# Performance work log

Measured on AMD Instinct MI355X. Metric: run time of the kernel, lower is better.

## Reference

```python
import jax, jax.numpy as jnp
import numpy as np

D_MODEL = 512
N_HEADS = 8
D_Q = 64   # d_queries == d_keys
D_V = 64
LN_EPS = 1e-5


def setup_inputs() -> dict:
    key = jax.random.key(0)
    ks = jax.random.split(key, 10)
    N, S = 4, 2048
    x = jax.random.normal(ks[0], (N, S, D_MODEL), dtype=jnp.float32)
    lengths = jax.random.randint(ks[1], (N,), 1, S + 1)  # true lengths in [1, S]
    s = 0.02
    Wq = jax.random.normal(ks[2], (D_MODEL, N_HEADS * D_Q), dtype=jnp.float32) * s
    bq = jnp.zeros((N_HEADS * D_Q,), dtype=jnp.float32)
    Wkv = jax.random.normal(ks[3], (D_MODEL, N_HEADS * (D_Q + D_V)), dtype=jnp.float32) * s
    bkv = jnp.zeros((N_HEADS * (D_Q + D_V),), dtype=jnp.float32)
    Wo = jax.random.normal(ks[4], (N_HEADS * D_V, D_MODEL), dtype=jnp.float32) * s
    bo = jnp.zeros((D_MODEL,), dtype=jnp.float32)
    gamma = jnp.ones((D_MODEL,), dtype=jnp.float32)
    beta = jnp.zeros((D_MODEL,), dtype=jnp.float32)
    return {"x": x, "key_value_sequence_lengths": lengths, "Wq": Wq, "bq": bq,
            "Wkv": Wkv, "bkv": bkv, "Wo": Wo, "bo": bo, "gamma": gamma, "beta": beta}


def reference(x, key_value_sequence_lengths, Wq, bq, Wkv, bkv, Wo, bo, gamma, beta):
    # Decoder self-attention: query_sequences == key_value_sequences == x.
    N, S, _ = x.shape
    H, dq, dv = N_HEADS, D_Q, D_V

    residual = x
    # Pre-LayerNorm (applied to both queries and keys/values since self-attention)
    mu = jnp.mean(x, axis=-1, keepdims=True)
    var = jnp.var(x, axis=-1, keepdims=True)
    xn = (x - mu) * jax.lax.rsqrt(var + LN_EPS) * gamma + beta

    q = (xn @ Wq + bq).reshape(N, S, H, dq).transpose(0, 2, 1, 3)          # (N,H,S,dq)
    kv = xn @ Wkv + bkv
    k = kv[..., : H * dq].reshape(N, S, H, dq).transpose(0, 2, 1, 3)       # (N,H,S,dq)
    v = kv[..., H * dq :].reshape(N, S, H, dv).transpose(0, 2, 1, 3)       # (N,H,S,dv)

    scores = jnp.einsum("nhqd,nhkd->nhqk", q, k) / jnp.sqrt(jnp.float32(dq))  # (N,H,S,S)

    # Padding mask over keys + causal (not-future) mask
    key_pos = jnp.arange(S)
    pad_ok = key_pos[None, None, None, :] < key_value_sequence_lengths[:, None, None, None]
    causal_ok = (key_pos[None, :] <= jnp.arange(S)[:, None])[None, None, :, :]
    mask = pad_ok & causal_ok
    scores = jnp.where(mask, scores, -jnp.inf)

    attn = jax.nn.softmax(scores, axis=-1)
    out = jnp.einsum("nhqk,nhkd->nqhd", attn, v).reshape(N, S, H * dv)
    out = out @ Wo + bo
    return out + residual
```

## Files before the change

kernel.cpp:

```cpp
#include <hip/hip_runtime.h>
#include <hip/hip_bf16.h>

typedef __attribute__((ext_vector_type(4))) float f32x4;
typedef __attribute__((ext_vector_type(16))) float f32x16;
typedef __attribute__((ext_vector_type(8))) short short8;

#define D_MODEL 512
#define SQ 2048
#define NH 8
#define NBATCH 4
#define MROWS (NBATCH * SQ)

#define CHUNKS_PER_NH 72
#define NSLOTS (32 * CHUNKS_PER_NH)

__device__ __forceinline__ ushort f2b(float x) {
  unsigned int u = __float_as_uint(x);
  return (ushort)((u + 0x7fffu + ((u >> 16) & 1u)) >> 16);
}

__device__ __forceinline__ f32x4 mfma16(short8 a, short8 b, f32x4 c) {
  return __builtin_amdgcn_mfma_f32_16x16x32_bf16(a, b, c, 0, 0, 0);
}
__device__ __forceinline__ f32x16 mfma32(short8 a, short8 b, f32x16 c) {
  return __builtin_amdgcn_mfma_f32_32x32x16_bf16(a, b, c, 0, 0, 0);
}

#define GLOAD_LDS16(g, l)                                                      \
  __builtin_amdgcn_global_load_lds(                                            \
      (const __attribute__((address_space(1))) unsigned int*)(g),              \
      (__attribute__((address_space(3))) unsigned int*)(l), 16, 0, 0)

__global__ __launch_bounds__(256) void transpose_w(const float* __restrict__ W,
                                                   ushort* __restrict__ WT,
                                                   int K, int N) {
  __shared__ ushort tile[32][33];
  int n0 = blockIdx.x * 32, k0 = blockIdx.y * 32;
  int tx = threadIdx.x & 31, ty = threadIdx.x >> 5;
#pragma unroll
  for (int i = 0; i < 4; ++i) {
    int k = ty + i * 8;
    tile[tx][k] = f2b(W[(size_t)(k0 + k) * N + n0 + tx]);
  }
  __syncthreads();
#pragma unroll
  for (int i = 0; i < 4; ++i) {
    int nn = ty + i * 8;
    WT[(size_t)(n0 + nn) * K + k0 + tx] = tile[nn][tx];
  }
}

__global__ __launch_bounds__(256) void ln_kernel(const float* __restrict__ x,
                                                 const float* __restrict__ gamma,
                                                 const float* __restrict__ beta,
                                                 ushort* __restrict__ xn) {
  int wid = threadIdx.x >> 6, lane = threadIdx.x & 63;
  int row = blockIdx.x * 4 + wid;
  const float4* xr = (const float4*)(x + (size_t)row * D_MODEL);
  float4 v0 = xr[lane];
  float4 v1 = xr[lane + 64];
  float s = v0.x + v0.y + v0.z + v0.w + v1.x + v1.y + v1.z + v1.w;
  float q = v0.x * v0.x + v0.y * v0.y + v0.z * v0.z + v0.w * v0.w +
            v1.x * v1.x + v1.y * v1.y + v1.z * v1.z + v1.w * v1.w;
#pragma unroll
  for (int m = 1; m < 64; m <<= 1) {
    s += __shfl_xor(s, m, 64);
    q += __shfl_xor(q, m, 64);
  }
  float mu = s * (1.f / 512.f);
  float var = q * (1.f / 512.f) - mu * mu;
  float rs = rsqrtf(var + 1e-5f);
  const float4* g4 = (const float4*)gamma;
  const float4* b4 = (const float4*)beta;
  ushort* out = xn + (size_t)row * D_MODEL;
#pragma unroll
  for (int i = 0; i < 2; ++i) {
    float4 v = i ? v1 : v0;
    float4 gg = g4[lane + i * 64];
    float4 bb = b4[lane + i * 64];
    ushort4 o;
    o.x = f2b((v.x - mu) * rs * gg.x + bb.x);
    o.y = f2b((v.y - mu) * rs * gg.y + bb.y);
    o.z = f2b((v.z - mu) * rs * gg.z + bb.z);
    o.w = f2b((v.w - mu) * rs * gg.w + bb.w);
    *(ushort4*)(out + (lane + i * 64) * 4) = o;
  }
}

__global__ __launch_bounds__(256) void qkv_gemm(
    const ushort* __restrict__ A, const ushort* __restrict__ BT,
    const float* __restrict__ bq, const float* __restrict__ bkv,
    ushort* __restrict__ qbuf, ushort* __restrict__ kvbuf, float qscale) {
  __shared__ __align__(16) ushort As[128 * 32];
  __shared__ __align__(16) ushort Bs[128 * 32];
  const int tid = threadIdx.x, lane = tid & 63, wid = tid >> 6;
  const int g = lane >> 4, r = lane & 15;
  const int wr = wid >> 1, wc = wid & 1;
  const int bm = blockIdx.y * 128, bn = blockIdx.x * 128;

  f32x4 acc[4][4];
#pragma unroll
  for (int a = 0; a < 4; ++a)
#pragma unroll
    for (int b = 0; b < 4; ++b) acc[a][b] = (f32x4){0.f, 0.f, 0.f, 0.f};

  const int srow = 32 * wid + (lane >> 2);
  const int scol = (lane & 3) * 8;
  const ushort* ga = A + (size_t)(bm + srow) * 512 + scol;
  const ushort* gb = BT + (size_t)(bn + srow) * 512 + scol;
  ushort* la = As + 32 * 32 * wid;
  ushort* lb = Bs + 32 * 32 * wid;

  for (int kb = 0; kb < 512; kb += 32) {
    __syncthreads();
    GLOAD_LDS16(ga + kb, la);
    GLOAD_LDS16(ga + kb + 16 * 512, la + 16 * 32);
    GLOAD_LDS16(gb + kb, lb);
    GLOAD_LDS16(gb + kb + 16 * 512, lb + 16 * 32);
    __syncthreads();
    short8 af[4], bf[4];
#pragma unroll
    for (int i2 = 0; i2 < 4; ++i2) {
      af[i2] = *(const short8*)&As[(wr * 64 + i2 * 16 + r) * 32 + g * 8];
      bf[i2] = *(const short8*)&Bs[(wc * 64 + i2 * 16 + r) * 32 + g * 8];
    }
#pragma unroll
    for (int a = 0; a < 4; ++a)
#pragma unroll
      for (int b = 0; b < 4; ++b) acc[a][b] = mfma16(af[a], bf[b], acc[a][b]);
  }

  const bool isQ = (bn < 512);
  const float* bias = isQ ? bq : bkv;
  ushort* dst = isQ ? qbuf : kvbuf;
  const int cb = isQ ? bn : bn - 512;
  const size_t stride = isQ ? 512 : 1024;
  const float scale = isQ ? qscale : 1.0f;

#pragma unroll
  for (int a = 0; a < 4; ++a) {
#pragma unroll
    for (int reg = 0; reg < 4; ++reg) {
      int row = bm + wr * 64 + a * 16 + g * 4 + reg;
#pragma unroll
      for (int b = 0; b < 4; ++b) {
        int col = cb + wc * 64 + b * 16 + r;
        dst[(size_t)row * stride + col] = f2b((acc[a][b][reg] + bias[col]) * scale);
      }
    }
  }
}

__global__ __launch_bounds__(256) void o_gemm(
    const ushort* __restrict__ A, const ushort* __restrict__ BT,
    const float* __restrict__ bias, const float* __restrict__ resid,
    float* __restrict__ outF) {
  __shared__ __align__(16) ushort As[128 * 32];
  __shared__ __align__(16) ushort Bs[128 * 32];
  const int tid = threadIdx.x, lane = tid & 63, wid = tid >> 6;
  const int g = lane >> 4, r = lane & 15;
  const int wr = wid >> 1, wc = wid & 1;
  const int bm = blockIdx.y * 128, bn = blockIdx.x * 128;

  f32x4 acc[4][4];
#pragma unroll
  for (int a = 0; a < 4; ++a)
#pragma unroll
    for (int b = 0; b < 4; ++b) acc[a][b] = (f32x4){0.f, 0.f, 0.f, 0.f};

  const int srow = 32 * wid + (lane >> 2);
  const int scol = (lane & 3) * 8;
  const ushort* ga = A + (size_t)(bm + srow) * 512 + scol;
  const ushort* gb = BT + (size_t)(bn + srow) * 512 + scol;
  ushort* la = As + 32 * 32 * wid;
  ushort* lb = Bs + 32 * 32 * wid;

  for (int kb = 0; kb < 512; kb += 32) {
    __syncthreads();
    GLOAD_LDS16(ga + kb, la);
    GLOAD_LDS16(ga + kb + 16 * 512, la + 16 * 32);
    GLOAD_LDS16(gb + kb, lb);
    GLOAD_LDS16(gb + kb + 16 * 512, lb + 16 * 32);
    __syncthreads();
    short8 af[4], bf[4];
#pragma unroll
    for (int i2 = 0; i2 < 4; ++i2) {
      af[i2] = *(const short8*)&As[(wr * 64 + i2 * 16 + r) * 32 + g * 8];
      bf[i2] = *(const short8*)&Bs[(wc * 64 + i2 * 16 + r) * 32 + g * 8];
    }
#pragma unroll
    for (int a = 0; a < 4; ++a)
#pragma unroll
      for (int b = 0; b < 4; ++b) acc[a][b] = mfma16(af[a], bf[b], acc[a][b]);
  }

#pragma unroll
  for (int a = 0; a < 4; ++a) {
#pragma unroll
    for (int reg = 0; reg < 4; ++reg) {
      int row = bm + wr * 64 + a * 16 + g * 4 + reg;
#pragma unroll
      for (int b = 0; b < 4; ++b) {
        int col = bn + wc * 64 + b * 16 + r;
        outF[(size_t)row * 512 + col] =
            acc[a][b][reg] + bias[col] + resid[(size_t)row * 512 + col];
      }
    }
  }
}

__global__ __launch_bounds__(256) void attn_kernel(
    const ushort* __restrict__ qbuf, const ushort* __restrict__ kvbuf,
    const int* __restrict__ lengths, ushort* __restrict__ partialO,
    float2* __restrict__ mlbuf) {
  __shared__ __align__(16) ushort smem[9728];

  const int tid = threadIdx.x, lane = tid & 63, wid = tid >> 6;
  const int l31 = lane & 31, h = lane >> 5;

  const int bid = blockIdx.x;
  const int xcd = bid & 7;
  const int j = bid >> 3;
  const int grp = j / 72;
  const int L = j - grp * 72;
  const int nh = (grp << 3) | xcd;
  const int n = nh >> 3, head = nh & 7;
  int qi = 0, c = L;
  while (c >= ((qi + 2) >> 1)) { c -= (qi + 2) >> 1; ++qi; }
  const int T = 4 * qi + 4, nch = (qi + 2) >> 1;
  const int t0 = (c * T) / nch;
  const int t1 = ((c + 1) * T) / nch;
  const int slot = nh * CHUNKS_PER_NH + L;

  const int qb = qi * 128;
  const int len = lengths[n];
  const int q0w = qb + 32 * wid;
  const int q_own = q0w + l31;
  const int nt_w_abs = 4 * qi + wid + 1;
  const int tlen = (len + 31) >> 5;
  int nt = min(t1, tlen) - t0;
  if (nt < 0) nt = 0;

  f32x16 o0, o1;
#pragma unroll
  for (int i = 0; i < 16; ++i) { o0[i] = 0.f; o1[i] = 0.f; }
  float m_ = -1e30f, ls = 0.f;

  const int skey = tid >> 3, sc8 = tid & 7;
  const int kp = lane & 15, dvb = wid * 4 + (lane >> 4);
  const int mu = (l31 >> 2) & 3;

  int voff[4];
#pragma unroll
  for (int jj = 0; jj < 4; ++jj) {
    int dv = 4 * dvb + jj;
    voff[jj] = dv * 20 + (((kp >> 2) ^ ((dv >> 2) & 3)) << 2) + (kp & 3);
  }

  const ushort* kvbase = kvbuf + (size_t)n * SQ * 1024 + head * 64;
  const ushort* kSrc = kvbase + (size_t)(t0 * 32 + skey) * 1024 + sc8 * 8;
  const ushort* vSrc = kvbase + 512 + (size_t)(t0 * 32 + 2 * kp) * 1024 + dvb * 4;
  const int kLdsOff = skey * 72 + sc8 * 8;

  if (nt > 0) {
    short8 qf[4];
    {
      const ushort* qp = qbuf + (size_t)(n * SQ + q_own) * 512 + head * 64 + 8 * h;
#pragma unroll
      for (int kc = 0; kc < 4; ++kc) qf[kc] = *(const short8*)(qp + 16 * kc);
    }

    uint4 kA, kB = {};
    uint2 vaA, vbA, vaB = {}, vbB = {};
    kA = *(const uint4*)kSrc;
    vaA = *(const uint2*)vSrc;
    vbA = *(const uint2*)(vSrc + 1024);
    kSrc += 32 * 1024;
    vSrc += 32 * 1024;
    if (nt > 1) {
      kB = *(const uint4*)kSrc;
      vaB = *(const uint2*)vSrc;
      vbB = *(const uint2*)(vSrc + 1024);
      kSrc += 32 * 1024;
      vSrc += 32 * 1024;
    }
    {
      *(uint4*)(smem + kLdsOff) = kA;
      const ushort* a16 = (const ushort*)&vaA;
      const ushort* b16 = (const ushort*)&vbA;
#pragma unroll
      for (int jj = 0; jj < 4; ++jj)
        ((unsigned*)(smem + 4608))[voff[jj]] =
            (unsigned)a16[jj] | ((unsigned)b16[jj] << 16);
    }
    __syncthreads();

    for (int i = 0; i < nt; ++i) {
      const int t = t0 + i;
      const int cur = i & 1;
      if (i + 2 < nt) {
        if (cur == 0) {
          kA = *(const uint4*)kSrc;
          vaA = *(const uint2*)vSrc;
          vbA = *(const uint2*)(vSrc + 1024);
        } else {
          kB = *(const uint4*)kSrc;
          vaB = *(const uint2*)vSrc;
          vbB = *(const uint2*)(vSrc + 1024);
        }
        kSrc += 32 * 1024;
        vSrc += 32 * 1024;
      }

      if (t < nt_w_abs) {
        const int kb = t * 32;
        const ushort* KtB = smem + cur * 2304;
        const ushort* VtB = smem + 4608 + cur * 2560;

        f32x16 s;
#pragma unroll
        for (int i2 = 0; i2 < 16; ++i2) s[i2] = 0.f;
        {
          const ushort* kr_ = KtB + l31 * 72 + 8 * h;
          short8 k0 = *(const short8*)(kr_);
          short8 k1 = *(const short8*)(kr_ + 16);
          short8 k2 = *(const short8*)(kr_ + 32);
          short8 k3 = *(const short8*)(kr_ + 48);
          s = mfma32(k0, qf[0], s);
          s = mfma32(k1, qf[1], s);
          s = mfma32(k2, qf[2], s);
          s = mfma32(k3, qf[3], s);
        }

        if (kb + 31 > q0w || kb + 31 >= len) {
          int keyb = kb + 4 * h;
#pragma unroll
          for (int reg = 0; reg < 16; ++reg) {
            int key = keyb + (reg & 3) + 8 * (reg >> 2);
            bool ok = (key <= q_own) && (key < len);
            s[reg] = ok ? s[reg] : -1e30f;
          }
        }

        float a0 = fmaxf(fmaxf(s[0], s[1]), s[2]);
        float a1 = fmaxf(fmaxf(s[3], s[4]), s[5]);
        float a2 = fmaxf(fmaxf(s[6], s[7]), s[8]);
        float a3 = fmaxf(fmaxf(s[9], s[10]), s[11]);
        float a4 = fmaxf(fmaxf(s[12], s[13]), s[14]);
        float mx = fmaxf(fmaxf(fmaxf(a0, a1), s[15]),
                         fmaxf(fmaxf(a2, a3), a4));
        {
          auto rr = __builtin_amdgcn_permlane32_swap(__float_as_uint(mx),
                                                     __float_as_uint(mx), false, false);
          mx = fmaxf(__uint_as_float(((const unsigned*)&rr)[0]),
                     __uint_as_float(((const unsigned*)&rr)[1]));
        }

        if (!__all(mx <= m_ + 8.0f)) {
          float mn = fmaxf(m_, mx);
          float sf = __builtin_amdgcn_exp2f(m_ - mn);
          m_ = mn;
          ls *= sf;
#pragma unroll
          for (int i2 = 0; i2 < 16; ++i2) { o0[i2] *= sf; o1[i2] *= sf; }
        }

        float p[16];
#pragma unroll
        for (int reg = 0; reg < 16; ++reg)
          p[reg] = __builtin_amdgcn_exp2f(s[reg] - m_);

        float rsum = ((p[0] + p[1]) + (p[2] + p[3])) + ((p[4] + p[5]) + (p[6] + p[7])) +
                     ((p[8] + p[9]) + (p[10] + p[11])) +
                     ((p[12] + p[13]) + (p[14] + p[15]));
        {
          auto rr = __builtin_amdgcn_permlane32_swap(__float_as_uint(rsum),
                                                     __float_as_uint(rsum), false, false);
          rsum = __uint_as_float(((const unsigned*)&rr)[0]) +
                 __uint_as_float(((const unsigned*)&rr)[1]);
        }
        ls += rsum;

        unsigned pk[8];
#pragma unroll
        for (int jj = 0; jj < 8; ++jj)
          pk[jj] = __builtin_amdgcn_perm(__float_as_uint(p[2 * jj + 1]),
                                         __float_as_uint(p[2 * jj]), 0x07060302u);

#pragma unroll
        for (int kc = 0; kc < 2; ++kc) {
          short8 pf;
          ((unsigned*)&pf)[0] = pk[4 * kc + 0];
          ((unsigned*)&pf)[1] = pk[4 * kc + 1];
          ((unsigned*)&pf)[2] = pk[4 * kc + 2];
          ((unsigned*)&pf)[3] = pk[4 * kc + 3];
          const int u0 = ((2 * kc) ^ mu) << 3;
          const ushort* vb0 = VtB + l31 * 40 + 4 * h;
          const ushort* vb1 = VtB + (32 + l31) * 40 + 4 * h;
          short8 vf0, vf1;
          ((uint2*)&vf0)[0] = *(const uint2*)(vb0 + u0);
          ((uint2*)&vf0)[1] = *(const uint2*)(vb0 + (u0 ^ 8));
          ((uint2*)&vf1)[0] = *(const uint2*)(vb1 + u0);
          ((uint2*)&vf1)[1] = *(const uint2*)(vb1 + (u0 ^ 8));
          o0 = mfma32(vf0, pf, o0);
          o1 = mfma32(vf1, pf, o1);
        }
      }

      if (i + 1 < nt) {
        ushort* KtN = smem + (cur ^ 1) * 2304;
        unsigned* VtN = (unsigned*)(smem + 4608 + (cur ^ 1) * 2560);
        if (cur == 0) {
          *(uint4*)(KtN + kLdsOff) = kB;
          const ushort* a16 = (const ushort*)&vaB;
          const ushort* b16 = (const ushort*)&vbB;
#pragma unroll
          for (int jj = 0; jj < 4; ++jj)
            VtN[voff[jj]] = (unsigned)a16[jj] | ((unsigned)b16[jj] << 16);
        } else {
          *(uint4*)(KtN + kLdsOff) = kA;
          const ushort* a16 = (const ushort*)&vaA;
          const ushort* b16 = (const ushort*)&vbA;
#pragma unroll
          for (int jj = 0; jj < 4; ++jj)
            VtN[voff[jj]] = (unsigned)a16[jj] | ((unsigned)b16[jj] << 16);
        }
      }
      __syncthreads();
    }
  }

  const unsigned long long alive = __ballot(ls > 0.f);
  {
    float inv = (ls > 0.f) ? 1.f / ls : 0.f;
    ushort* OtW = smem + wid * (32 * 68);
#pragma unroll
    for (int b = 0; b < 2; ++b) {
#pragma unroll
      for (int reg = 0; reg < 16; reg += 2) {
        float e0 = (b ? o1[reg] : o0[reg]) * inv;
        float e1 = (b ? o1[reg + 1] : o0[reg + 1]) * inv;
        unsigned pko = __builtin_amdgcn_perm(__float_as_uint(e1),
                                             __float_as_uint(e0), 0x07060302u);
        int dv = 32 * b + (reg & 3) + 8 * (reg >> 2) + 4 * h;
        *(unsigned*)(OtW + l31 * 68 + dv) = pko;
      }
    }
    if (h == 0) mlbuf[slot * 128 + 32 * wid + l31] = make_float2(m_, ls);
  }
  __syncthreads();
  if (alive) {
    int r = lane >> 1, sg = lane & 1;
    if ((alive >> r) & 1ULL) {
      const ushort* rp = smem + wid * (32 * 68) + r * 68 + sg * 32;
      uint2 d0 = *(const uint2*)(rp);
      uint2 d1 = *(const uint2*)(rp + 4);
      uint2 d2 = *(const uint2*)(rp + 8);
      uint2 d3 = *(const uint2*)(rp + 12);
      uint2 d4 = *(const uint2*)(rp + 16);
      uint2 d5 = *(const uint2*)(rp + 20);
      uint2 d6 = *(const uint2*)(rp + 24);
      uint2 d7 = *(const uint2*)(rp + 28);
      ushort* gp = partialO + (size_t)slot * 8192 + (32 * wid + r) * 64 + sg * 32;
      *(uint4*)(gp) = make_uint4(d0.x, d0.y, d1.x, d1.y);
      *(uint4*)(gp + 8) = make_uint4(d2.x, d2.y, d3.x, d3.y);
      *(uint4*)(gp + 16) = make_uint4(d4.x, d4.y, d5.x, d5.y);
      *(uint4*)(gp + 24) = make_uint4(d6.x, d6.y, d7.x, d7.y);
    }
  }
}

__global__ __launch_bounds__(256) void attn_combine(
    const ushort* __restrict__ partialO, const float2* __restrict__ mlbuf,
    ushort* __restrict__ attout) {
  const int bx = blockIdx.x;
  const int nh = bx >> 4, qi = bx & 15;
  const int nch = (qi + 2) >> 1;
  const int off = (qi * (qi + 2) + (qi & 1)) >> 2;
  const int n = nh >> 3, head = nh & 7;
  const int slot0 = nh * CHUNKS_PER_NH + off;

  const int tid = threadIdx.x;
  const int r = tid >> 1, half = tid & 1;

  float mstar = -1e30f;
  for (int c = 0; c < nch; ++c) {
    float2 ml = mlbuf[(slot0 + c) * 128 + r];
    mstar = fmaxf(mstar, ml.x);
  }

  float acc[32];
#pragma unroll
  for (int j = 0; j < 32; ++j) acc[j] = 0.f;
  float Lsum = 0.f;

  for (int c = 0; c < nch; ++c) {
    float2 ml = mlbuf[(slot0 + c) * 128 + r];
    if (ml.y > 0.f) {
      float cf = ml.y * __builtin_amdgcn_exp2f(ml.x - mstar);
      Lsum += cf;
      const uint4* p =
          (const uint4*)(partialO + (size_t)(slot0 + c) * 8192 + r * 64 + half * 32);
#pragma unroll
      for (int u = 0; u < 4; ++u) {
        uint4 d = p[u];
        unsigned w[4] = {d.x, d.y, d.z, d.w};
#pragma unroll
        for (int k = 0; k < 4; ++k) {
          acc[u * 8 + 2 * k] += cf * __uint_as_float(w[k] << 16);
          acc[u * 8 + 2 * k + 1] += cf * __uint_as_float(w[k] & 0xffff0000u);
        }
      }
    }
  }

  const float inv = 1.f / Lsum;
  uint4 outw[4];
#pragma unroll
  for (int u = 0; u < 4; ++u) {
    unsigned ww[4];
#pragma unroll
    for (int k = 0; k < 4; ++k) {
      float e0 = acc[u * 8 + 2 * k] * inv;
      float e1 = acc[u * 8 + 2 * k + 1] * inv;
      ww[k] = ((unsigned)f2b(e0)) | (((unsigned)f2b(e1)) << 16);
    }
    outw[u] = make_uint4(ww[0], ww[1], ww[2], ww[3]);
  }
  ushort* gp = attout + (size_t)(n * SQ + qi * 128 + r) * 512 + head * 64 + half * 32;
#pragma unroll
  for (int u = 0; u < 4; ++u) ((uint4*)gp)[u] = outw[u];
}

extern "C" void kernel_launch(void* const* d_in, const int* in_sizes, int n_in,
                              void* d_out, int out_size, void* d_ws, size_t ws_size,
                              hipStream_t stream) {
  const float* x = (const float*)d_in[0];
  const int* lens = (const int*)d_in[1];
  const float* Wq = (const float*)d_in[2];
  const float* bq = (const float*)d_in[3];
  const float* Wkv = (const float*)d_in[4];
  const float* bkv = (const float*)d_in[5];
  const float* Wo = (const float*)d_in[6];
  const float* bo = (const float*)d_in[7];
  const float* gamma = (const float*)d_in[8];
  const float* beta = (const float*)d_in[9];
  float* out = (float*)d_out;

  size_t off = 0;
  auto alloc = [&](size_t bytes) {
    void* p = (char*)d_ws + off;
    off += (bytes + 255) & ~(size_t)255;
    return p;
  };
  ushort* xn = (ushort*)alloc((size_t)MROWS * 512 * 2);
  ushort* qbuf = (ushort*)alloc((size_t)MROWS * 512 * 2);
  ushort* kvbuf = (ushort*)alloc((size_t)MROWS * 1024 * 2);
  ushort* WT = (ushort*)alloc((size_t)1536 * 512 * 2);
  ushort* WoT = (ushort*)alloc((size_t)512 * 512 * 2);
  ushort* partialO = (ushort*)alloc((size_t)NSLOTS * 8192 * 2);
  float2* mlbuf = (float2*)alloc((size_t)NSLOTS * 128 * 8);
  ushort* attout = xn;

  transpose_w<<<dim3(16, 16), 256, 0, stream>>>(Wq, WT, 512, 512);
  transpose_w<<<dim3(32, 16), 256, 0, stream>>>(Wkv, WT + 512 * 512, 512, 1024);
  transpose_w<<<dim3(16, 16), 256, 0, stream>>>(Wo, WoT, 512, 512);

  ln_kernel<<<MROWS / 4, 256, 0, stream>>>(x, gamma, beta, xn);

  qkv_gemm<<<dim3(12, 64), 256, 0, stream>>>(xn, WT, bq, bkv, qbuf, kvbuf,
                                             0.125f * 1.44269504f);

  attn_kernel<<<dim3(NSLOTS), 256, 0, stream>>>(qbuf, kvbuf, lens, partialO, mlbuf);
  attn_combine<<<dim3(512), 256, 0, stream>>>(partialO, mlbuf, attout);

  o_gemm<<<dim3(4, 64), 256, 0, stream>>>(attout, WoT, bo, x, out);
}
```

Measured before the change: 123.9 us.

## Load K fragments directly from global into registers, bypassing LDS staging

```diff
diff --git a/kernel.cpp b/kernel.cpp
--- a/kernel.cpp
+++ b/kernel.cpp
@@ -213,7 +213,7 @@
     const ushort* __restrict__ qbuf, const ushort* __restrict__ kvbuf,
     const int* __restrict__ lengths, ushort* __restrict__ partialO,
     float2* __restrict__ mlbuf) {
-  __shared__ __align__(16) ushort smem[9728];
+  __shared__ __align__(16) ushort smem[8704];
 
   const int tid = threadIdx.x, lane = tid & 63, wid = tid >> 6;
   const int l31 = lane & 31, h = lane >> 5;
@@ -246,7 +246,6 @@
   for (int i = 0; i < 16; ++i) { o0[i] = 0.f; o1[i] = 0.f; }
   float m_ = -1e30f, ls = 0.f;
 
-  const int skey = tid >> 3, sc8 = tid & 7;
   const int kp = lane & 15, dvb = wid * 4 + (lane >> 4);
   const int mu = (l31 >> 2) & 3;
 
@@ -258,9 +257,8 @@
   }
 
   const ushort* kvbase = kvbuf + (size_t)n * SQ * 1024 + head * 64;
-  const ushort* kSrc = kvbase + (size_t)(t0 * 32 + skey) * 1024 + sc8 * 8;
+  const ushort* kRow = kvbase + (size_t)(t0 * 32 + l31) * 1024 + 8 * h;
   const ushort* vSrc = kvbase + 512 + (size_t)(t0 * 32 + 2 * kp) * 1024 + dvb * 4;
-  const int kLdsOff = skey * 72 + sc8 * 8;
 
   if (nt > 0) {
     short8 qf[4];
@@ -270,27 +268,20 @@
       for (int kc = 0; kc < 4; ++kc) qf[kc] = *(const short8*)(qp + 16 * kc);
     }
 
-    uint4 kA, kB = {};
-    uint2 vaA, vbA, vaB = {}, vbB = {};
-    kA = *(const uint4*)kSrc;
-    vaA = *(const uint2*)vSrc;
-    vbA = *(const uint2*)(vSrc + 1024);
-    kSrc += 32 * 1024;
+    short8 kfA[4], kfB[4];
+    uint2 va, vb;
+#pragma unroll
+    for (int kc = 0; kc < 4; ++kc) kfA[kc] = *(const short8*)(kRow + 16 * kc);
+    kRow += 32 * 1024;
+    va = *(const uint2*)vSrc;
+    vb = *(const uint2*)(vSrc + 1024);
     vSrc += 32 * 1024;
-    if (nt > 1) {
-      kB = *(const uint4*)kSrc;
-      vaB = *(const uint2*)vSrc;
-      vbB = *(const uint2*)(vSrc + 1024);
-      kSrc += 32 * 1024;
-      vSrc += 32 * 1024;
-    }
     {
-      *(uint4*)(smem + kLdsOff) = kA;
-      const ushort* a16 = (const ushort*)&vaA;
-      const ushort* b16 = (const ushort*)&vbA;
+      const ushort* a16 = (const ushort*)&va;
+      const ushort* b16 = (const ushort*)&vb;
 #pragma unroll
       for (int jj = 0; jj < 4; ++jj)
-        ((unsigned*)(smem + 4608))[voff[jj]] =
+        ((unsigned*)smem)[voff[jj]] =
             (unsigned)a16[jj] | ((unsigned)b16[jj] << 16);
     }
     __syncthreads();
@@ -298,39 +289,31 @@
     for (int i = 0; i < nt; ++i) {
       const int t = t0 + i;
       const int cur = i & 1;
-      if (i + 2 < nt) {
-        if (cur == 0) {
-          kA = *(const uint4*)kSrc;
-          vaA = *(const uint2*)vSrc;
-          vbA = *(const uint2*)(vSrc + 1024);
-        } else {
-          kB = *(const uint4*)kSrc;
-          vaB = *(const uint2*)vSrc;
-          vbB = *(const uint2*)(vSrc + 1024);
-        }
-        kSrc += 32 * 1024;
+      const bool more = (i + 1 < nt);
+      uint2 va2, vb2;
+      if (more) {
+        va2 = *(const uint2*)vSrc;
+        vb2 = *(const uint2*)(vSrc + 1024);
         vSrc += 32 * 1024;
+        if (t + 1 < nt_w_abs) {
+#pragma unroll
+          for (int kc = 0; kc < 4; ++kc)
+            kfB[kc] = *(const short8*)(kRow + 16 * kc);
+        }
+        kRow += 32 * 1024;
       }
 
       if (t < nt_w_abs) {
         const int kb = t * 32;
-        const ushort* KtB = smem + cur * 2304;
-        const ushort* VtB = smem + 4608 + cur * 2560;
+        const ushort* VtB = smem + cur * 2560;
 
         f32x16 s;
 #pragma unroll
         for (int i2 = 0; i2 < 16; ++i2) s[i2] = 0.f;
-        {
-          const ushort* kr_ = KtB + l31 * 72 + 8 * h;
-          short8 k0 = *(const short8*)(kr_);
-          short8 k1 = *(const short8*)(kr_ + 16);
-          short8 k2 = *(const short8*)(kr_ + 32);
-          short8 k3 = *(const short8*)(kr_ + 48);
-          s = mfma32(k0, qf[0], s);
-          s = mfma32(k1, qf[1], s);
-          s = mfma32(k2, qf[2], s);
-          s = mfma32(k3, qf[3], s);
-        }
+        s = mfma32(kfA[0], qf[0], s);
+        s = mfma32(kfA[1], qf[1], s);
+        s = mfma32(kfA[2], qf[2], s);
+        s = mfma32(kfA[3], qf[3], s);
 
         if (kb + 31 > q0w || kb + 31 >= len) {
           int keyb = kb + 4 * h;
@@ -407,24 +390,15 @@
         }
       }
 
-      if (i + 1 < nt) {
-        ushort* KtN = smem + (cur ^ 1) * 2304;
-        unsigned* VtN = (unsigned*)(smem + 4608 + (cur ^ 1) * 2560);
-        if (cur == 0) {
-          *(uint4*)(KtN + kLdsOff) = kB;
-          const ushort* a16 = (const ushort*)&vaB;
-          const ushort* b16 = (const ushort*)&vbB;
-#pragma unroll
-          for (int jj = 0; jj < 4; ++jj)
-            VtN[voff[jj]] = (unsigned)a16[jj] | ((unsigned)b16[jj] << 16);
-        } else {
-          *(uint4*)(KtN + kLdsOff) = kA;
-          const ushort* a16 = (const ushort*)&vaA;
-          const ushort* b16 = (const ushort*)&vbA;
-#pragma unroll
-          for (int jj = 0; jj < 4; ++jj)
-            VtN[voff[jj]] = (unsigned)a16[jj] | ((unsigned)b16[jj] << 16);
-        }
+      if (more) {
+        unsigned* VtN = (unsigned*)smem + (cur ^ 1) * 1280;
+        const ushort* a16 = (const ushort*)&va2;
+        const ushort* b16 = (const ushort*)&vb2;
+#pragma unroll
+        for (int jj = 0; jj < 4; ++jj)
+          VtN[voff[jj]] = (unsigned)a16[jj] | ((unsigned)b16[jj] << 16);
+#pragma unroll
+        for (int kc = 0; kc < 4; ++kc) kfA[kc] = kfB[kc];
       }
       __syncthreads();
     }
```

Measured after the change: 142.2 us. 14.8% more time.

## Process two KV tiles per attention loop iteration with doubled LDS staging

Applied to the files above, without the earlier changes.

```diff
diff --git a/kernel.cpp b/kernel.cpp
--- a/kernel.cpp
+++ b/kernel.cpp
@@ -213,7 +213,7 @@
     const ushort* __restrict__ qbuf, const ushort* __restrict__ kvbuf,
     const int* __restrict__ lengths, ushort* __restrict__ partialO,
     float2* __restrict__ mlbuf) {
-  __shared__ __align__(16) ushort smem[9728];
+  __shared__ __align__(16) ushort smem[19456];
 
   const int tid = threadIdx.x, lane = tid & 63, wid = tid >> 6;
   const int l31 = lane & 31, h = lane >> 5;
@@ -227,9 +227,9 @@
   const int n = nh >> 3, head = nh & 7;
   int qi = 0, c = L;
   while (c >= ((qi + 2) >> 1)) { c -= (qi + 2) >> 1; ++qi; }
-  const int T = 4 * qi + 4, nch = (qi + 2) >> 1;
-  const int t0 = (c * T) / nch;
-  const int t1 = ((c + 1) * T) / nch;
+  const int P = 2 * qi + 2, nch = (qi + 2) >> 1;
+  const int t0 = 2 * ((c * P) / nch);
+  const int t1 = 2 * (((c + 1) * P) / nch);
   const int slot = nh * CHUNKS_PER_NH + L;
 
   const int qb = qi * 128;
@@ -240,6 +240,7 @@
   const int tlen = (len + 31) >> 5;
   int nt = min(t1, tlen) - t0;
   if (nt < 0) nt = 0;
+  const int np = (nt + 1) >> 1;
 
   f32x16 o0, o1;
 #pragma unroll
@@ -270,66 +271,212 @@
       for (int kc = 0; kc < 4; ++kc) qf[kc] = *(const short8*)(qp + 16 * kc);
     }
 
-    uint4 kA, kB = {};
-    uint2 vaA, vbA, vaB = {}, vbB = {};
-    kA = *(const uint4*)kSrc;
+    uint4 kra, krb;
+    uint2 vaA, vbA, vaB, vbB;
+    kra = *(const uint4*)kSrc;
+    krb = *(const uint4*)(kSrc + 32 * 1024);
     vaA = *(const uint2*)vSrc;
     vbA = *(const uint2*)(vSrc + 1024);
-    kSrc += 32 * 1024;
-    vSrc += 32 * 1024;
-    if (nt > 1) {
-      kB = *(const uint4*)kSrc;
-      vaB = *(const uint2*)vSrc;
-      vbB = *(const uint2*)(vSrc + 1024);
-      kSrc += 32 * 1024;
-      vSrc += 32 * 1024;
-    }
+    vaB = *(const uint2*)(vSrc + 32 * 1024);
+    vbB = *(const uint2*)(vSrc + 33 * 1024);
+    kSrc += 64 * 1024;
+    vSrc += 64 * 1024;
     {
-      *(uint4*)(smem + kLdsOff) = kA;
+      *(uint4*)(smem + kLdsOff) = kra;
+      *(uint4*)(smem + 2304 + kLdsOff) = krb;
+      unsigned* V0 = (unsigned*)(smem + 9216);
+      unsigned* V1 = V0 + 1280;
       const ushort* a16 = (const ushort*)&vaA;
       const ushort* b16 = (const ushort*)&vbA;
-#pragma unroll
-      for (int jj = 0; jj < 4; ++jj)
-        ((unsigned*)(smem + 4608))[voff[jj]] =
-            (unsigned)a16[jj] | ((unsigned)b16[jj] << 16);
+      const ushort* c16 = (const ushort*)&vaB;
+      const ushort* d16 = (const ushort*)&vbB;
+#pragma unroll
+      for (int jj = 0; jj < 4; ++jj) {
+        V0[voff[jj]] = (unsigned)a16[jj] | ((unsigned)b16[jj] << 16);
+        V1[voff[jj]] = (unsigned)c16[jj] | ((unsigned)d16[jj] << 16);
+      }
     }
     __syncthreads();
 
-    for (int i = 0; i < nt; ++i) {
-      const int t = t0 + i;
+    for (int i = 0; i < np; ++i) {
+      const int tA = t0 + 2 * i, tB = tA + 1;
       const int cur = i & 1;
-      if (i + 2 < nt) {
-        if (cur == 0) {
-          kA = *(const uint4*)kSrc;
-          vaA = *(const uint2*)vSrc;
-          vbA = *(const uint2*)(vSrc + 1024);
-        } else {
-          kB = *(const uint4*)kSrc;
-          vaB = *(const uint2*)vSrc;
-          vbB = *(const uint2*)(vSrc + 1024);
-        }
-        kSrc += 32 * 1024;
-        vSrc += 32 * 1024;
+      const bool more = (i + 1 < np);
+      if (more) {
+        kra = *(const uint4*)kSrc;
+        krb = *(const uint4*)(kSrc + 32 * 1024);
+        vaA = *(const uint2*)vSrc;
+        vbA = *(const uint2*)(vSrc + 1024);
+        vaB = *(const uint2*)(vSrc + 32 * 1024);
+        vbB = *(const uint2*)(vSrc + 33 * 1024);
+        kSrc += 64 * 1024;
+        vSrc += 64 * 1024;
       }
-
-      if (t < nt_w_abs) {
-        const int kb = t * 32;
-        const ushort* KtB = smem + cur * 2304;
-        const ushort* VtB = smem + 4608 + cur * 2560;
-
+      const bool condA = (tA < nt_w_abs);
+      const bool condB = (tB < nt_w_abs) && (2 * i + 1 < nt);
+      const ushort* KtA = smem + cur * 4608;
+      const ushort* KtB = KtA + 2304;
+      const ushort* VtA = smem + 9216 + cur * 5120;
+      const ushort* VtB = VtA + 2560;
+
+      if (condB) {
+        const int kbA = tA * 32, kbB = kbA + 32;
+        f32x16 s, s2;
+#pragma unroll
+        for (int i2 = 0; i2 < 16; ++i2) { s[i2] = 0.f; s2[i2] = 0.f; }
+        {
+          const ushort* krA_ = KtA + l31 * 72 + 8 * h;
+          const ushort* krB_ = KtB + l31 * 72 + 8 * h;
+          short8 a0 = *(const short8*)(krA_);
+          short8 a1 = *(const short8*)(krA_ + 16);
+          short8 a2 = *(const short8*)(krA_ + 32);
+          short8 a3 = *(const short8*)(krA_ + 48);
+          short8 b0 = *(const short8*)(krB_);
+          short8 b1 = *(const short8*)(krB_ + 16);
+          short8 b2 = *(const short8*)(krB_ + 32);
+          short8 b3 = *(const short8*)(krB_ + 48);
+          __builtin_amdgcn_s_setprio(1);
+          s = mfma32(a0, qf[0], s);
+          s2 = mfma32(b0, qf[0], s2);
+          s = mfma32(a1, qf[1], s);
+          s2 = mfma32(b1, qf[1], s2);
+          s = mfma32(a2, qf[2], s);
+          s2 = mfma32(b2, qf[2], s2);
+          s = mfma32(a3, qf[3], s);
+          s2 = mfma32(b3, qf[3], s2);
+          __builtin_amdgcn_s_setprio(0);
+        }
+
+        if (kbA + 31 > q0w || kbA + 31 >= len) {
+          int keyb = kbA + 4 * h;
+#pragma unroll
+          for (int reg = 0; reg < 16; ++reg) {
+            int key = keyb + (reg & 3) + 8 * (reg >> 2);
+            bool ok = (key <= q_own) && (key < len);
+            s[reg] = ok ? s[reg] : -1e30f;
+          }
+        }
+        if (kbB + 31 > q0w || kbB + 31 >= len) {
+          int keyb = kbB + 4 * h;
+#pragma unroll
+          for (int reg = 0; reg < 16; ++reg) {
+            int key = keyb + (reg & 3) + 8 * (reg >> 2);
+            bool ok = (key <= q_own) && (key < len);
+            s2[reg] = ok ? s2[reg] : -1e30f;
+          }
+        }
+
+        float m0 = fmaxf(fmaxf(s[0], s[1]), fmaxf(s[2], s[3]));
+        float m1 = fmaxf(fmaxf(s[4], s[5]), fmaxf(s[6], s[7]));
+        float m2 = fmaxf(fmaxf(s[8], s[9]), fmaxf(s[10], s[11]));
+        float m3 = fmaxf(fmaxf(s[12], s[13]), fmaxf(s[14], s[15]));
+        float m4 = fmaxf(fmaxf(s2[0], s2[1]), fmaxf(s2[2], s2[3]));
+        float m5 = fmaxf(fmaxf(s2[4], s2[5]), fmaxf(s2[6], s2[7]));
+        float m6 = fmaxf(fmaxf(s2[8], s2[9]), fmaxf(s2[10], s2[11]));
+        float m7 = fmaxf(fmaxf(s2[12], s2[13]), fmaxf(s2[14], s2[15]));
+        float mx = fmaxf(fmaxf(fmaxf(m0, m1), fmaxf(m2, m3)),
+                         fmaxf(fmaxf(m4, m5), fmaxf(m6, m7)));
+        {
+          auto rr = __builtin_amdgcn_permlane32_swap(__float_as_uint(mx),
+                                                     __float_as_uint(mx), false, false);
+          mx = fmaxf(__uint_as_float(((const unsigned*)&rr)[0]),
+                     __uint_as_float(((const unsigned*)&rr)[1]));
+        }
+
+        if (!__all(mx <= m_ + 8.0f)) {
+          float mn = fmaxf(m_, mx);
+          float sf = __builtin_amdgcn_exp2f(m_ - mn);
+          m_ = mn;
+          ls *= sf;
+#pragma unroll
+          for (int i2 = 0; i2 < 16; ++i2) { o0[i2] *= sf; o1[i2] *= sf; }
+        }
+
+#pragma unroll
+        for (int reg = 0; reg < 16; ++reg) {
+          s[reg] = __builtin_amdgcn_exp2f(s[reg] - m_);
+          s2[reg] = __builtin_amdgcn_exp2f(s2[reg] - m_);
+        }
+
+        float rsum = (((s[0] + s[1]) + (s[2] + s[3])) + ((s[4] + s[5]) + (s[6] + s[7]))) +
+                     (((s[8] + s[9]) + (s[10] + s[11])) +
+                      ((s[12] + s[13]) + (s[14] + s[15]))) +
+                     (((s2[0] + s2[1]) + (s2[2] + s2[3])) +
+                      ((s2[4] + s2[5]) + (s2[6] + s2[7]))) +
+                     (((s2[8] + s2[9]) + (s2[10] + s2[11])) +
+                      ((s2[12] + s2[13]) + (s2[14] + s2[15])));
+        {
+          auto rr = __builtin_amdgcn_permlane32_swap(__float_as_uint(rsum),
+                                                     __float_as_uint(rsum), false, false);
+          rsum = __uint_as_float(((const unsigned*)&rr)[0]) +
+                 __uint_as_float(((const unsigned*)&rr)[1]);
+        }
+        ls += rsum;
+
+        unsigned pkA[8], pkB[8];
+#pragma unroll
+        for (int jj = 0; jj < 8; ++jj) {
+          pkA[jj] = __builtin_amdgcn_perm(__float_as_uint(s[2 * jj + 1]),
+                                          __float_as_uint(s[2 * jj]), 0x07060302u);
+          pkB[jj] = __builtin_amdgcn_perm(__float_as_uint(s2[2 * jj + 1]),
+                                          __float_as_uint(s2[2 * jj]), 0x07060302u);
+        }
+
+        __builtin_amdgcn_s_setprio(1);
+#pragma unroll
+        for (int kc = 0; kc < 2; ++kc) {
+          short8 pf;
+          ((unsigned*)&pf)[0] = pkA[4 * kc + 0];
+          ((unsigned*)&pf)[1] = pkA[4 * kc + 1];
+          ((unsigned*)&pf)[2] = pkA[4 * kc + 2];
+          ((unsigned*)&pf)[3] = pkA[4 * kc + 3];
+          const int u0 = ((2 * kc) ^ mu) << 3;
+          const ushort* vb0 = VtA + l31 * 40 + 4 * h;
+          const ushort* vb1 = VtA + (32 + l31) * 40 + 4 * h;
+          short8 vf0, vf1;
+          ((uint2*)&vf0)[0] = *(const uint2*)(vb0 + u0);
+          ((uint2*)&vf0)[1] = *(const uint2*)(vb0 + (u0 ^ 8));
+          ((uint2*)&vf1)[0] = *(const uint2*)(vb1 + u0);
+          ((uint2*)&vf1)[1] = *(const uint2*)(vb1 + (u0 ^ 8));
+          o0 = mfma32(vf0, pf, o0);
+          o1 = mfma32(vf1, pf, o1);
+        }
+#pragma unroll
+        for (int kc = 0; kc < 2; ++kc) {
+          short8 pf;
+          ((unsigned*)&pf)[0] = pkB[4 * kc + 0];
+          ((unsigned*)&pf)[1] = pkB[4 * kc + 1];
+          ((unsigned*)&pf)[2] = pkB[4 * kc + 2];
+          ((unsigned*)&pf)[3] = pkB[4 * kc + 3];
+          const int u0 = ((2 * kc) ^ mu) << 3;
+          const ushort* vb0 = VtB + l31 * 40 + 4 * h;
+          const ushort* vb1 = VtB + (32 + l31) * 40 + 4 * h;
+          short8 vf0, vf1;
+          ((uint2*)&vf0)[0] = *(const uint2*)(vb0 + u0);
+          ((uint2*)&vf0)[1] = *(const uint2*)(vb0 + (u0 ^ 8));
+          ((uint2*)&vf1)[0] = *(const uint2*)(vb1 + u0);
+          ((uint2*)&vf1)[1] = *(const uint2*)(vb1 + (u0 ^ 8));
+          o0 = mfma32(vf0, pf, o0);
+          o1 = mfma32(vf1, pf, o1);
+        }
+        __builtin_amdgcn_s_setprio(0);
+      } else if (condA) {
+        const int kb = tA * 32;
         f32x16 s;
 #pragma unroll
         for (int i2 = 0; i2 < 16; ++i2) s[i2] = 0.f;
         {
-          const ushort* kr_ = KtB + l31 * 72 + 8 * h;
+          const ushort* kr_ = KtA + l31 * 72 + 8 * h;
           short8 k0 = *(const short8*)(kr_);
           short8 k1 = *(const short8*)(kr_ + 16);
           short8 k2 = *(const short8*)(kr_ + 32);
           short8 k3 = *(const short8*)(kr_ + 48);
+          __builtin_amdgcn_s_setprio(1);
           s = mfma32(k0, qf[0], s);
           s = mfma32(k1, qf[1], s);
           s = mfma32(k2, qf[2], s);
           s = mfma32(k3, qf[3], s);
+          __builtin_amdgcn_s_setprio(0);
         }
 
         if (kb + 31 > q0w || kb + 31 >= len) {
@@ -365,14 +512,13 @@
           for (int i2 = 0; i2 < 16; ++i2) { o0[i2] *= sf; o1[i2] *= sf; }
         }
 
-        float p[16];
 #pragma unroll
         for (int reg = 0; reg < 16; ++reg)
-          p[reg] = __builtin_amdgcn_exp2f(s[reg] - m_);
-
-        float rsum = ((p[0] + p[1]) + (p[2] + p[3])) + ((p[4] + p[5]) + (p[6] + p[7])) +
-                     ((p[8] + p[9]) + (p[10] + p[11])) +
-                     ((p[12] + p[13]) + (p[14] + p[15]));
+          s[reg] = __builtin_amdgcn_exp2f(s[reg] - m_);
+
+        float rsum = ((s[0] + s[1]) + (s[2] + s[3])) + ((s[4] + s[5]) + (s[6] + s[7])) +
+                     ((s[8] + s[9]) + (s[10] + s[11])) +
+                     ((s[12] + s[13]) + (s[14] + s[15]));
         {
           auto rr = __builtin_amdgcn_permlane32_swap(__float_as_uint(rsum),
                                                      __float_as_uint(rsum), false, false);
@@ -384,9 +530,10 @@
         unsigned pk[8];
 #pragma unroll
         for (int jj = 0; jj < 8; ++jj)
-          pk[jj] = __builtin_amdgcn_perm(__float_as_uint(p[2 * jj + 1]),
-                                         __float_as_uint(p[2 * jj]), 0x07060302u);
-
+          pk[jj] = __builtin_amdgcn_perm(__float_as_uint(s[2 * jj + 1]),
+                                         __float_as_uint(s[2 * jj]), 0x07060302u);
+
+        __builtin_amdgcn_s_setprio(1);
 #pragma unroll
         for (int kc = 0; kc < 2; ++kc) {
           short8 pf;
@@ -395,8 +542,8 @@
           ((unsigned*)&pf)[2] = pk[4 * kc + 2];
           ((unsigned*)&pf)[3] = pk[4 * kc + 3];
           const int u0 = ((2 * kc) ^ mu) << 3;
-          const ushort* vb0 = VtB + l31 * 40 + 4 * h;
-          const ushort* vb1 = VtB + (32 + l31) * 40 + 4 * h;
+          const ushort* vb0 = VtA + l31 * 40 + 4 * h;
+          const ushort* vb1 = VtA + (32 + l31) * 40 + 4 * h;
           short8 vf0, vf1;
           ((uint2*)&vf0)[0] = *(const uint2*)(vb0 + u0);
           ((uint2*)&vf0)[1] = *(const uint2*)(vb0 + (u0 ^ 8));
@@ -405,25 +552,23 @@
           o0 = mfma32(vf0, pf, o0);
           o1 = mfma32(vf1, pf, o1);
         }
+        __builtin_amdgcn_s_setprio(0);
       }
 
-      if (i + 1 < nt) {
-        ushort* KtN = smem + (cur ^ 1) * 2304;
-        unsigned* VtN = (unsigned*)(smem + 4608 + (cur ^ 1) * 2560);
-        if (cur == 0) {
-          *(uint4*)(KtN + kLdsOff) = kB;
-          const ushort* a16 = (const ushort*)&vaB;
-          const ushort* b16 = (const ushort*)&vbB;
-#pragma unroll
-          for (int jj = 0; jj < 4; ++jj)
-            VtN[voff[jj]] = (unsigned)a16[jj] | ((unsigned)b16[jj] << 16);
-        } else {
-          *(uint4*)(KtN + kLdsOff) = kA;
-          const ushort* a16 = (const ushort*)&vaA;
-          const ushort* b16 = (const ushort*)&vbA;
-#pragma unroll
-          for (int jj = 0; jj < 4; ++jj)
-            VtN[voff[jj]] = (unsigned)a16[jj] | ((unsigned)b16[jj] << 16);
+      if (more) {
+        ushort* KN = smem + (cur ^ 1) * 4608;
+        *(uint4*)(KN + kLdsOff) = kra;
+        *(uint4*)(KN + 2304 + kLdsOff) = krb;
+        unsigned* VN0 = (unsigned*)(smem + 9216 + (cur ^ 1) * 5120);
+        unsigned* VN1 = VN0 + 1280;
+        const ushort* a16 = (const ushort*)&vaA;
+        const ushort* b16 = (const ushort*)&vbA;
+        const ushort* c16 = (const ushort*)&vaB;
+        const ushort* d16 = (const ushort*)&vbB;
+#pragma unroll
+        for (int jj = 0; jj < 4; ++jj) {
+          VN0[voff[jj]] = (unsigned)a16[jj] | ((unsigned)b16[jj] << 16);
+          VN1[voff[jj]] = (unsigned)c16[jj] | ((unsigned)d16[jj] << 16);
         }
       }
       __syncthreads();
```

Result: slower. 126.9 us (+2.4%).

## Fuse split-KV combine into attention kernel via last-arriver atomic counter

Applied to the files above, without the earlier changes.

```diff
diff --git a/kernel.cpp b/kernel.cpp
--- a/kernel.cpp
+++ b/kernel.cpp
@@ -212,8 +212,10 @@
 __global__ __launch_bounds__(256) void attn_kernel(
     const ushort* __restrict__ qbuf, const ushort* __restrict__ kvbuf,
     const int* __restrict__ lengths, ushort* __restrict__ partialO,
-    float2* __restrict__ mlbuf) {
+    float2* __restrict__ mlbuf, ushort* __restrict__ attout,
+    int* __restrict__ ctr) {
   __shared__ __align__(16) ushort smem[9728];
+  __shared__ int sOld;
 
   const int tid = threadIdx.x, lane = tid & 63, wid = tid >> 6;
   const int l31 = lane & 31, h = lane >> 5;
@@ -326,10 +328,12 @@
           short8 k1 = *(const short8*)(kr_ + 16);
           short8 k2 = *(const short8*)(kr_ + 32);
           short8 k3 = *(const short8*)(kr_ + 48);
+          __builtin_amdgcn_s_setprio(1);
           s = mfma32(k0, qf[0], s);
           s = mfma32(k1, qf[1], s);
           s = mfma32(k2, qf[2], s);
           s = mfma32(k3, qf[3], s);
+          __builtin_amdgcn_s_setprio(0);
         }
 
         if (kb + 31 > q0w || kb + 31 >= len) {
@@ -387,6 +391,7 @@
           pk[jj] = __builtin_amdgcn_perm(__float_as_uint(p[2 * jj + 1]),
                                          __float_as_uint(p[2 * jj]), 0x07060302u);
 
+        __builtin_amdgcn_s_setprio(1);
 #pragma unroll
         for (int kc = 0; kc < 2; ++kc) {
           short8 pf;
@@ -405,6 +410,7 @@
           o0 = mfma32(vf0, pf, o0);
           o1 = mfma32(vf1, pf, o1);
         }
+        __builtin_amdgcn_s_setprio(0);
       }
 
       if (i + 1 < nt) {
@@ -446,9 +452,31 @@
         *(unsigned*)(OtW + l31 * 68 + dv) = pko;
       }
     }
-    if (h == 0) mlbuf[slot * 128 + 32 * wid + l31] = make_float2(m_, ls);
+    if (h == 0 && nch > 1)
+      mlbuf[slot * 128 + 32 * wid + l31] = make_float2(m_, ls);
   }
   __syncthreads();
+
+  if (nch == 1) {
+    int r = lane >> 1, sg = lane & 1;
+    const ushort* rp = smem + wid * (32 * 68) + r * 68 + sg * 32;
+    uint2 d0 = *(const uint2*)(rp);
+    uint2 d1 = *(const uint2*)(rp + 4);
+    uint2 d2 = *(const uint2*)(rp + 8);
+    uint2 d3 = *(const uint2*)(rp + 12);
+    uint2 d4 = *(const uint2*)(rp + 16);
+    uint2 d5 = *(const uint2*)(rp + 20);
+    uint2 d6 = *(const uint2*)(rp + 24);
+    uint2 d7 = *(const uint2*)(rp + 28);
+    ushort* gp = attout + (size_t)(n * SQ + qb + 32 * wid + r) * 512 +
+                 head * 64 + sg * 32;
+    *(uint4*)(gp) = make_uint4(d0.x, d0.y, d1.x, d1.y);
+    *(uint4*)(gp + 8) = make_uint4(d2.x, d2.y, d3.x, d3.y);
+    *(uint4*)(gp + 16) = make_uint4(d4.x, d4.y, d5.x, d5.y);
+    *(uint4*)(gp + 24) = make_uint4(d6.x, d6.y, d7.x, d7.y);
+    return;
+  }
+
   if (alive) {
     int r = lane >> 1, sg = lane & 1;
     if ((alive >> r) & 1ULL) {
@@ -468,68 +496,65 @@
       *(uint4*)(gp + 24) = make_uint4(d6.x, d6.y, d7.x, d7.y);
     }
   }
-}
-
-__global__ __launch_bounds__(256) void attn_combine(
-    const ushort* __restrict__ partialO, const float2* __restrict__ mlbuf,
-    ushort* __restrict__ attout) {
-  const int bx = blockIdx.x;
-  const int nh = bx >> 4, qi = bx & 15;
-  const int nch = (qi + 2) >> 1;
-  const int off = (qi * (qi + 2) + (qi & 1)) >> 2;
-  const int n = nh >> 3, head = nh & 7;
-  const int slot0 = nh * CHUNKS_PER_NH + off;
-
-  const int tid = threadIdx.x;
-  const int r = tid >> 1, half = tid & 1;
-
-  float mstar = -1e30f;
-  for (int c = 0; c < nch; ++c) {
-    float2 ml = mlbuf[(slot0 + c) * 128 + r];
-    mstar = fmaxf(mstar, ml.x);
-  }
-
-  float acc[32];
-#pragma unroll
-  for (int j = 0; j < 32; ++j) acc[j] = 0.f;
-  float Lsum = 0.f;
-
-  for (int c = 0; c < nch; ++c) {
-    float2 ml = mlbuf[(slot0 + c) * 128 + r];
-    if (ml.y > 0.f) {
-      float cf = ml.y * __builtin_amdgcn_exp2f(ml.x - mstar);
-      Lsum += cf;
-      const uint4* p =
-          (const uint4*)(partialO + (size_t)(slot0 + c) * 8192 + r * 64 + half * 32);
-#pragma unroll
-      for (int u = 0; u < 4; ++u) {
-        uint4 d = p[u];
-        unsigned w[4] = {d.x, d.y, d.z, d.w};
+
+  __syncthreads();
+  if (tid == 0) {
+    __threadfence();
+    sOld = atomicAdd(&ctr[nh * 16 + qi], 1);
+  }
+  __syncthreads();
+  if (sOld != nch - 1) return;
+  __threadfence();
+
+  {
+    const int slot0 = slot - c;
+    const int r = tid >> 1, half = tid & 1;
+    float mstar = -1e30f;
+    for (int cc = 0; cc < nch; ++cc)
+      mstar = fmaxf(mstar, mlbuf[(slot0 + cc) * 128 + r].x);
+
+    ushort* gp = attout + (size_t)(n * SQ + qi * 128 + r) * 512 +
+                 head * 64 + half * 32;
+#pragma unroll
+    for (int pass = 0; pass < 2; ++pass) {
+      float acc[16];
+#pragma unroll
+      for (int k = 0; k < 16; ++k) acc[k] = 0.f;
+      float Lsum = 0.f;
+      for (int cc = 0; cc < nch; ++cc) {
+        float2 ml = mlbuf[(slot0 + cc) * 128 + r];
+        if (ml.y > 0.f) {
+          float cf = ml.y * __builtin_amdgcn_exp2f(ml.x - mstar);
+          Lsum += cf;
+          const uint4* p = (const uint4*)(partialO + (size_t)(slot0 + cc) * 8192 +
+                                          r * 64 + half * 32 + pass * 16);
+#pragma unroll
+          for (int u = 0; u < 2; ++u) {
+            uint4 d = p[u];
+            unsigned w[4] = {d.x, d.y, d.z, d.w};
+#pragma unroll
+            for (int k = 0; k < 4; ++k) {
+              acc[u * 8 + 2 * k] += cf * __uint_as_float(w[k] << 16);
+              acc[u * 8 + 2 * k + 1] += cf * __uint_as_float(w[k] & 0xffff0000u);
+            }
+          }
+        }
+      }
+      const float inv = 1.f / Lsum;
+      ushort* gpp = gp + pass * 16;
+#pragma unroll
+      for (int u = 0; u < 2; ++u) {
+        unsigned ww[4];
 #pragma unroll
         for (int k = 0; k < 4; ++k) {
-          acc[u * 8 + 2 * k] += cf * __uint_as_float(w[k] << 16);
-          acc[u * 8 + 2 * k + 1] += cf * __uint_as_float(w[k] & 0xffff0000u);
-        }
-      }
-    }
-  }
-
-  const float inv = 1.f / Lsum;
-  uint4 outw[4];
-#pragma unroll
-  for (int u = 0; u < 4; ++u) {
-    unsigned ww[4];
-#pragma unroll
-    for (int k = 0; k < 4; ++k) {
-      float e0 = acc[u * 8 + 2 * k] * inv;
-      float e1 = acc[u * 8 + 2 * k + 1] * inv;
-      ww[k] = ((unsigned)f2b(e0)) | (((unsigned)f2b(e1)) << 16);
-    }
-    outw[u] = make_uint4(ww[0], ww[1], ww[2], ww[3]);
-  }
-  ushort* gp = attout + (size_t)(n * SQ + qi * 128 + r) * 512 + head * 64 + half * 32;
-#pragma unroll
-  for (int u = 0; u < 4; ++u) ((uint4*)gp)[u] = outw[u];
+          float e0 = acc[u * 8 + 2 * k] * inv;
+          float e1 = acc[u * 8 + 2 * k + 1] * inv;
+          ww[k] = ((unsigned)f2b(e0)) | (((unsigned)f2b(e1)) << 16);
+        }
+        ((uint4*)gpp)[u] = make_uint4(ww[0], ww[1], ww[2], ww[3]);
+      }
+    }
+  }
 }
 
 extern "C" void kernel_launch(void* const* d_in, const int* in_sizes, int n_in,
@@ -560,7 +585,10 @@
   ushort* WoT = (ushort*)alloc((size_t)512 * 512 * 2);
   ushort* partialO = (ushort*)alloc((size_t)NSLOTS * 8192 * 2);
   float2* mlbuf = (float2*)alloc((size_t)NSLOTS * 128 * 8);
+  int* ctr = (int*)alloc(512 * sizeof(int));
   ushort* attout = xn;
+
+  hipMemsetAsync(ctr, 0, 512 * sizeof(int), stream);
 
   transpose_w<<<dim3(16, 16), 256, 0, stream>>>(Wq, WT, 512, 512);
   transpose_w<<<dim3(32, 16), 256, 0, stream>>>(Wkv, WT + 512 * 512, 512, 1024);
@@ -571,8 +599,8 @@
   qkv_gemm<<<dim3(12, 64), 256, 0, stream>>>(xn, WT, bq, bkv, qbuf, kvbuf,
                                              0.125f * 1.44269504f);
 
-  attn_kernel<<<dim3(NSLOTS), 256, 0, stream>>>(qbuf, kvbuf, lens, partialO, mlbuf);
-  attn_combine<<<dim3(512), 256, 0, stream>>>(partialO, mlbuf, attout);
+  attn_kernel<<<dim3(NSLOTS), 256, 0, stream>>>(qbuf, kvbuf, lens, partialO,
+                                                mlbuf, attout, ctr);
 
   o_gemm<<<dim3(4, 64), 256, 0, stream>>>(attout, WoT, bo, x, out);
 }
```

Result: slower. 267.2 us (+115.7%).
